# Performance work log

Hardware: AMD Instinct MI355X
Metric: run time of the kernel (lower is better)

## Reference

```python
import jax, jax.numpy as jnp
import numpy as np

N_NODES = 100000
N_CELLS = 200000
N_EDGES = 300000
D = 128            # input_size == attention_size
HID = 128          # hidden width of custom_func MLP
SCALE = np.sqrt(np.float32(D))


def segment_softmax(src, seg_ids, num_segments):
    # src: [M, 1], seg_ids: [M] -> softmax normalized within each segment
    m = jax.ops.segment_max(src, seg_ids, num_segments=num_segments)
    e = jnp.exp(src - m[seg_ids])
    s = jax.ops.segment_sum(e, seg_ids, num_segments=num_segments)
    return e / s[seg_ids]


def setup_inputs() -> dict:
    key = jax.random.key(0)
    ks = jax.random.split(key, 9)
    cell_attr = jax.random.normal(ks[0], (N_CELLS, D), dtype=jnp.float32)
    edge_attr = jax.random.normal(ks[1], (N_EDGES, D), dtype=jnp.float32)
    node_embedding = jax.random.normal(ks[2], (N_NODES, D), dtype=jnp.float32)
    edge_index = jax.random.randint(ks[3], (2, N_EDGES), 0, N_NODES, dtype=jnp.int32)
    face = jax.random.randint(ks[4], (3, N_CELLS), 0, N_NODES, dtype=jnp.int32)
    # custom_func: 2-layer MLP (2D -> HID -> D)
    W1 = jax.random.normal(ks[5], (2 * D, HID), dtype=jnp.float32) / np.sqrt(2 * D)
    b1 = jnp.zeros((HID,), dtype=jnp.float32)
    W2 = jax.random.normal(ks[6], (HID, D), dtype=jnp.float32) / np.sqrt(HID)
    b2 = jnp.zeros((D,), dtype=jnp.float32)
    return {"cell_attr": cell_attr, "edge_attr": edge_attr,
            "node_embedding": node_embedding, "edge_index": edge_index,
            "face": face, "W1": W1, "b1": b1, "W2": W2, "b2": b2}


def reference(cell_attr, edge_attr, node_embedding, edge_index, face, W1, b1, W2, b2):
    senders, receivers = edge_index[0], edge_index[1]
    two_out = jnp.concatenate([receivers, senders], axis=0)   # outdegree order [2E]
    two_edge = jnp.concatenate([edge_attr, edge_attr], axis=0)  # [2E, D]

    # attention over edges grouped by target (outdegree) node
    att_src = jnp.sum(two_edge * node_embedding[two_out], axis=1, keepdims=True) / SCALE
    att = segment_softmax(att_src, two_out, N_NODES)            # [2E, 1]
    node_agg = jax.ops.segment_sum(two_edge * att, two_out, num_segments=N_NODES)  # [N, D]

    # cells gather mean of their 3 nodes
    cell_agg = (node_agg[face[0]] + node_agg[face[1]] + node_agg[face[2]]) / 3.0  # [C, D]

    # custom_func MLP on cat(cell_attr, cell_agg)
    h = jax.nn.relu(jnp.concatenate([cell_attr, cell_agg], axis=1) @ W1 + b1)
    cell_attr_new = h @ W2 + b2                                  # [C, D]

    # scatter_mean of cell features back to nodes
    cells_node_index = jnp.concatenate([face[0], face[1], face[2]], axis=0)  # [3C]
    tripled = jnp.concatenate([cell_attr_new] * 3, axis=0)                   # [3C, D]
    sums = jax.ops.segment_sum(tripled, cells_node_index, num_segments=N_NODES)
    counts = jax.ops.segment_sum(jnp.ones((3 * N_CELLS,), jnp.float32),
                                 cells_node_index, num_segments=N_NODES)
    node_attr = sums / jnp.maximum(counts, 1.0)[:, None]

    return cell_attr_new, node_attr
```

## Files before the change

kernel.cpp:

```cpp
#include <hip/hip_runtime.h>

#define NN 100000
#define NC 200000
#define NE 300000
#define D  128
#define NB 391
#define HB 2344

typedef unsigned short u16;
typedef __attribute__((ext_vector_type(8))) short bf16x8;
typedef __attribute__((ext_vector_type(4))) float f32x4;

__device__ __forceinline__ u16 f2bf(float x) {
    unsigned int u = __float_as_uint(x);
    u += 0x7fffu + ((u >> 16) & 1u);
    return (u16)(u >> 16);
}
__device__ __forceinline__ float bf2f(u16 h) {
    return __uint_as_float((unsigned int)h << 16);
}
__device__ __forceinline__ unsigned int cvt_pk_bf16(float a, float b) {
    unsigned int r;
    asm("v_cvt_pk_bf16_f32 %0, %1, %2" : "=v"(r) : "v"(a), "v"(b));
    return r;
}

#define MFMA16(a, b, c) __builtin_amdgcn_mfma_f32_16x16x32_bf16((a), (b), (c), 0, 0, 0)

__global__ __launch_bounds__(256) void k_hist_w(const int* __restrict__ ei,
                                                const int* __restrict__ face,
                                                int* __restrict__ cntA,
                                                int* __restrict__ cntF,
                                                const float* __restrict__ W1,
                                                const float* __restrict__ W2,
                                                u16* __restrict__ w1h, u16* __restrict__ w1l,
                                                u16* __restrict__ w2h, u16* __restrict__ w2l) {
    int b = blockIdx.x;
    int t = threadIdx.x;
    if (b < HB) {
        int i = b * 256 + t;
        if (i >= 2 * NE) return;
        int tgt = (i < NE) ? ei[NE + i] : ei[i - NE];
        atomicAdd(&cntA[tgt], 1);
    } else if (b < 2 * HB) {
        int i = (b - HB) * 256 + t;
        if (i >= 3 * NC) return;
        atomicAdd(&cntF[face[i]], 1);
    } else {
        int tid = (b - 2 * HB) * 256 + t;
        if (tid >= 6144) return;
        int l = tid & 63;
        int f = tid >> 6;
        const float* W; u16 *oh, *ol; int fi;
        if (f < 64) { W = W1; oh = w1h; ol = w1l; fi = f; }
        else        { W = W2; oh = w2h; ol = w2l; fi = f - 64; }
        int kt = fi >> 3, nt = fi & 7;
        int k0 = kt * 32 + 8 * (l >> 4);
        int n  = nt * 16 + (l & 15);
        #pragma unroll
        for (int i = 0; i < 8; i++) {
            float x = W[(size_t)(k0 + i) * 128 + n];
            u16 h = f2bf(x);
            oh[(size_t)fi * 512 + l * 8 + i] = h;
            ol[(size_t)fi * 512 + l * 8 + i] = f2bf(x - bf2f(h));
        }
    }
}

__global__ __launch_bounds__(256) void k_scan_blocks(const int* __restrict__ cntA,
                                                     const int* __restrict__ cntF,
                                                     int* __restrict__ bsumA,
                                                     int* __restrict__ bsumF) {
    __shared__ int s[256];
    int bb = blockIdx.x;
    bool fa = bb >= NB;
    const int* cnt = fa ? cntF : cntA;
    int* bsum = fa ? bsumF : bsumA;
    int blk = fa ? bb - NB : bb;
    int t = threadIdx.x;
    int i = blk * 256 + t;
    s[t] = (i < NN) ? cnt[i] : 0;
    __syncthreads();
    #pragma unroll
    for (int off = 128; off > 0; off >>= 1) {
        if (t < off) s[t] += s[t + off];
        __syncthreads();
    }
    if (t == 0) bsum[blk] = s[0];
}

__global__ __launch_bounds__(512) void k_scan_top(int* __restrict__ bsumA,
                                                  int* __restrict__ bsumF, int nb) {
    __shared__ int s[512];
    int* bsum = blockIdx.x ? bsumF : bsumA;
    int t = threadIdx.x;
    int v = (t < nb) ? bsum[t] : 0;
    s[t] = v;
    __syncthreads();
    #pragma unroll
    for (int off = 1; off < 512; off <<= 1) {
        int x = (t >= off) ? s[t - off] : 0;
        __syncthreads();
        s[t] += x;
        __syncthreads();
    }
    if (t < nb) bsum[t] = s[t] - v;
}

__global__ __launch_bounds__(256) void k_scan_final(const int* __restrict__ cntA,
                                                    const int* __restrict__ cntF,
                                                    const int* __restrict__ bsumA,
                                                    const int* __restrict__ bsumF,
                                                    int* __restrict__ offA,
                                                    int* __restrict__ offF) {
    __shared__ int s[256];
    int bb = blockIdx.x;
    bool fa = bb >= NB;
    const int* cnt = fa ? cntF : cntA;
    const int* bsum = fa ? bsumF : bsumA;
    int* off_out = fa ? offF : offA;
    int total = fa ? 3 * NC : 2 * NE;
    int blk = fa ? bb - NB : bb;
    int t = threadIdx.x;
    int i = blk * 256 + t;
    int v = (i < NN) ? cnt[i] : 0;
    s[t] = v;
    __syncthreads();
    #pragma unroll
    for (int off = 1; off < 256; off <<= 1) {
        int x = (t >= off) ? s[t - off] : 0;
        __syncthreads();
        s[t] += x;
        __syncthreads();
    }
    if (i < NN) off_out[i] = s[t] - v + bsum[blk];
    if (i == 0) off_out[NN] = total;
}

__global__ __launch_bounds__(256) void k_fill(const int* __restrict__ ei,
                                              const int* __restrict__ face,
                                              const int* __restrict__ offA,
                                              const int* __restrict__ offF,
                                              int* __restrict__ curA,
                                              int* __restrict__ curF,
                                              int* __restrict__ slotsA,
                                              int* __restrict__ slotsF) {
    int b = blockIdx.x;
    int t = threadIdx.x;
    if (b < HB) {
        int i = b * 256 + t;
        if (i >= 2 * NE) return;
        int tgt = (i < NE) ? ei[NE + i] : ei[i - NE];
        int pos = offA[tgt] + atomicAdd(&curA[tgt], 1);
        slotsA[pos] = (i < NE) ? i : i - NE;
    } else {
        int i = (b - HB) * 256 + t;
        if (i >= 3 * NC) return;
        int tgt = face[i];
        int pos = offF[tgt] + atomicAdd(&curF[tgt], 1);
        int c = i; if (c >= NC) c -= NC; if (c >= NC) c -= NC;
        slotsF[pos] = c;
    }
}

__global__ __launch_bounds__(256) void k_agg_att(const float* __restrict__ edge_attr,
                                                 const float* __restrict__ emb,
                                                 const int* __restrict__ offs,
                                                 const int* __restrict__ slots,
                                                 float* __restrict__ na) {
    int n = blockIdx.x * 4 + (threadIdx.x >> 6);
    int lane = threadIdx.x & 63;
    if (n >= NN) return;
    int s0 = offs[n], s1 = offs[n + 1];
    int deg = s1 - s0;
    float2 e = ((const float2*)(emb + (size_t)n * D))[lane];
    const float inv_scale = 0.08838834764831845f;
    float2 acc = {0.f, 0.f};
    float wsum = 0.f;
    int base = 0;
    while (base < deg) {
        int chunk = deg - base;
        if (chunk > 64) chunk = 64;
        int sl = (lane < chunk) ? slots[s0 + base + lane] : 0;
        int j = 0;
        for (; j + 4 <= chunk; j += 4) {
            int r0 = __shfl(sl, j),     r1 = __shfl(sl, j + 1);
            int r2 = __shfl(sl, j + 2), r3 = __shfl(sl, j + 3);
            float2 a0 = ((const float2*)(edge_attr + (size_t)r0 * D))[lane];
            float2 a1 = ((const float2*)(edge_attr + (size_t)r1 * D))[lane];
            float2 a2 = ((const float2*)(edge_attr + (size_t)r2 * D))[lane];
            float2 a3 = ((const float2*)(edge_attr + (size_t)r3 * D))[lane];
            float d0 = a0.x * e.x + a0.y * e.y;
            float d1 = a1.x * e.x + a1.y * e.y;
            float d2 = a2.x * e.x + a2.y * e.y;
            float d3 = a3.x * e.x + a3.y * e.y;
            #pragma unroll
            for (int off = 32; off > 0; off >>= 1) {
                d0 += __shfl_xor(d0, off);
                d1 += __shfl_xor(d1, off);
                d2 += __shfl_xor(d2, off);
                d3 += __shfl_xor(d3, off);
            }
            float w0 = __expf(d0 * inv_scale);
            float w1 = __expf(d1 * inv_scale);
            float w2 = __expf(d2 * inv_scale);
            float w3 = __expf(d3 * inv_scale);
            acc.x += w0 * a0.x + w1 * a1.x + w2 * a2.x + w3 * a3.x;
            acc.y += w0 * a0.y + w1 * a1.y + w2 * a2.y + w3 * a3.y;
            wsum += (w0 + w1) + (w2 + w3);
        }
        for (; j < chunk; ++j) {
            int rr = __shfl(sl, j);
            float2 a = ((const float2*)(edge_attr + (size_t)rr * D))[lane];
            float d = a.x * e.x + a.y * e.y;
            #pragma unroll
            for (int off = 32; off > 0; off >>= 1) d += __shfl_xor(d, off);
            float w = __expf(d * inv_scale);
            acc.x += w * a.x;
            acc.y += w * a.y;
            wsum += w;
        }
        base += chunk;
    }
    float inv = (deg > 0) ? 1.f / wsum : 0.f;
    float2 r; r.x = acc.x * inv; r.y = acc.y * inv;
    ((float2*)(na + (size_t)n * D))[lane] = r;
}

__global__ __launch_bounds__(256) void k_smean_gather(const float* __restrict__ cell_out,
                                                      const int* __restrict__ offs,
                                                      const int* __restrict__ slots,
                                                      float* __restrict__ node_out) {
    int n = blockIdx.x * 4 + (threadIdx.x >> 6);
    int lane = threadIdx.x & 63;
    if (n >= NN) return;
    int s0 = offs[n], s1 = offs[n + 1];
    int deg = s1 - s0;
    float2 acc = {0.f, 0.f};
    int base = 0;
    while (base < deg) {
        int chunk = deg - base;
        if (chunk > 64) chunk = 64;
        int sl = 0;
        if (lane < chunk) sl = slots[s0 + base + lane];
        int j = 0;
        for (; j + 4 <= chunk; j += 4) {
            int c0 = __shfl(sl, j),     c1 = __shfl(sl, j + 1);
            int c2 = __shfl(sl, j + 2), c3 = __shfl(sl, j + 3);
            float2 y0 = ((const float2*)(cell_out + (size_t)c0 * D))[lane];
            float2 y1 = ((const float2*)(cell_out + (size_t)c1 * D))[lane];
            float2 y2 = ((const float2*)(cell_out + (size_t)c2 * D))[lane];
            float2 y3 = ((const float2*)(cell_out + (size_t)c3 * D))[lane];
            acc.x += y0.x + y1.x + y2.x + y3.x;
            acc.y += y0.y + y1.y + y2.y + y3.y;
        }
        for (; j < chunk; ++j) {
            int cc = __shfl(sl, j);
            float2 y = ((const float2*)(cell_out + (size_t)cc * D))[lane];
            acc.x += y.x;
            acc.y += y.y;
        }
        base += chunk;
    }
    float inv = deg ? 1.f / (float)deg : 0.f;
    float2 r; r.x = acc.x * inv; r.y = acc.y * inv;
    ((float2*)(node_out + (size_t)n * D))[lane] = r;
}

__device__ __forceinline__ void stage_split(char* lds, int row, int col8, const float* v) {
    unsigned int byte = ((unsigned int)row << 9) + ((unsigned int)col8 << 4);
    byte ^= (unsigned int)(row & 7) << 4;
    uint4 hi, lo;
    unsigned int* hp = (unsigned int*)&hi;
    unsigned int* lp = (unsigned int*)&lo;
    #pragma unroll
    for (int i = 0; i < 4; i++) {
        unsigned int h = cvt_pk_bf16(v[2 * i], v[2 * i + 1]);
        float h0 = __uint_as_float(h << 16);
        float h1 = __uint_as_float(h & 0xffff0000u);
        hp[i] = h;
        lp[i] = cvt_pk_bf16(v[2 * i] - h0, v[2 * i + 1] - h1);
    }
    *(uint4*)(lds + byte)         = hi;
    *(uint4*)(lds + 16384 + byte) = lo;
}

__global__ __launch_bounds__(256, 5) void k_mlp(const float* __restrict__ cell_attr,
                                                const float* __restrict__ na,
                                                const int* __restrict__ face,
                                                const u16* __restrict__ w1h,
                                                const u16* __restrict__ w1l,
                                                const u16* __restrict__ w2h,
                                                const u16* __restrict__ w2l,
                                                const float* __restrict__ b1,
                                                const float* __restrict__ b2,
                                                float* __restrict__ out) {
    __shared__ char lds[32768];
    const int t  = threadIdx.x;
    const int c0 = blockIdx.x * 32;

    {
        const int r = t >> 3;
        const int q = t & 7;
        float v[16];
        const float* pa = cell_attr + (size_t)(c0 + r) * D + q * 16;
        #pragma unroll
        for (int i = 0; i < 4; i++) *(float4*)(v + 4 * i) = *(const float4*)(pa + 4 * i);
        stage_split(lds, r, q * 2,     v);
        stage_split(lds, r, q * 2 + 1, v + 8);

        const int cid = c0 + r;
        const int f0 = face[cid], f1 = face[NC + cid], f2 = face[2 * NC + cid];
        const float* p0 = na + (size_t)f0 * D + q * 16;
        const float* p1 = na + (size_t)f1 * D + q * 16;
        const float* p2 = na + (size_t)f2 * D + q * 16;
        const float third = 1.f / 3.f;
        #pragma unroll
        for (int i = 0; i < 4; i++) {
            float4 a0 = *(const float4*)(p0 + 4 * i);
            float4 a1 = *(const float4*)(p1 + 4 * i);
            float4 a2 = *(const float4*)(p2 + 4 * i);
            v[4 * i + 0] = (a0.x + a1.x + a2.x) * third;
            v[4 * i + 1] = (a0.y + a1.y + a2.y) * third;
            v[4 * i + 2] = (a0.z + a1.z + a2.z) * third;
            v[4 * i + 3] = (a0.w + a1.w + a2.w) * third;
        }
        stage_split(lds, r, 16 + q * 2, v);
        stage_split(lds, r, 17 + q * 2, v + 8);
    }
    __syncthreads();

    const int w  = t >> 6;
    const int l  = t & 63;
    const int lr = l & 15;
    const int lg = l >> 4;
    const unsigned int swz = (unsigned int)(lr & 7) << 4;
    const size_t wl8 = (size_t)l * 8;
    const f32x4 z4 = {0.f, 0.f, 0.f, 0.f};
    f32x4 acc[2][2] = {{z4, z4}, {z4, z4}};

    {
        const unsigned int abase = ((unsigned int)lr << 9) + ((unsigned int)lg << 4);
        const u16* pW1h = w1h + (size_t)(w * 2) * 512 + wl8;
        const u16* pW1l = w1l + (size_t)(w * 2) * 512 + wl8;
        #pragma unroll 2
        for (int kt = 0; kt < 8; ++kt) {
            unsigned int ab = (abase + (unsigned int)kt * 64) ^ swz;
            bf16x8 aH0 = *(const bf16x8*)(lds + ab);
            bf16x8 aL0 = *(const bf16x8*)(lds + 16384 + ab);
            bf16x8 aH1 = *(const bf16x8*)(lds + ab + 8192);
            bf16x8 aL1 = *(const bf16x8*)(lds + 16384 + ab + 8192);
            #pragma unroll
            for (int jn = 0; jn < 2; ++jn) {
                size_t fo = (size_t)(kt * 8 + jn) * 512;
                bf16x8 bH = *(const bf16x8*)(pW1h + fo);
                bf16x8 bL = *(const bf16x8*)(pW1l + fo);
                acc[0][jn] = MFMA16(aH0, bL, acc[0][jn]);
                acc[0][jn] = MFMA16(aL0, bH, acc[0][jn]);
                acc[0][jn] = MFMA16(aH0, bH, acc[0][jn]);
                acc[1][jn] = MFMA16(aH1, bL, acc[1][jn]);
                acc[1][jn] = MFMA16(aL1, bH, acc[1][jn]);
                acc[1][jn] = MFMA16(aH1, bH, acc[1][jn]);
            }
        }
    }

    __syncthreads();

    {
        const int col0 = w * 32 + lr;
        const int col1 = col0 + 16;
        const float bb0 = b1[col0];
        const float bb1 = b1[col1];
        #pragma unroll
        for (int rt = 0; rt < 2; ++rt) {
            #pragma unroll
            for (int r = 0; r < 4; ++r) {
                int row = rt * 16 + lg * 4 + r;
                float h0 = fmaxf(acc[rt][0][r] + bb0, 0.f);
                float h1 = fmaxf(acc[rt][1][r] + bb1, 0.f);
                unsigned int ph = cvt_pk_bf16(h0, h1);
                float f0 = __uint_as_float(ph << 16);
                float f1 = __uint_as_float(ph & 0xffff0000u);
                unsigned int pl = cvt_pk_bf16(h0 - f0, h1 - f1);
                unsigned int swzr = (unsigned int)(row & 7) << 4;
                unsigned int b0 = (((unsigned int)row << 8) + ((unsigned int)col0 << 1)) ^ swzr;
                unsigned int bcol1 = (((unsigned int)row << 8) + ((unsigned int)col1 << 1)) ^ swzr;
                *(u16*)(lds + b0)            = (u16)ph;
                *(u16*)(lds + bcol1)         = (u16)(ph >> 16);
                *(u16*)(lds + 8192 + b0)     = (u16)pl;
                *(u16*)(lds + 8192 + bcol1)  = (u16)(pl >> 16);
            }
        }
    }
    __syncthreads();

    f32x4 acc2[2][2] = {{z4, z4}, {z4, z4}};
    {
        const unsigned int abase = ((unsigned int)lr << 8) + ((unsigned int)lg << 4);
        const u16* pW2h = w2h + (size_t)(w * 2) * 512 + wl8;
        const u16* pW2l = w2l + (size_t)(w * 2) * 512 + wl8;
        #pragma unroll 2
        for (int kt = 0; kt < 4; ++kt) {
            unsigned int ab = (abase + (unsigned int)kt * 64) ^ swz;
            bf16x8 aH0 = *(const bf16x8*)(lds + ab);
            bf16x8 aL0 = *(const bf16x8*)(lds + 8192 + ab);
            bf16x8 aH1 = *(const bf16x8*)(lds + ab + 4096);
            bf16x8 aL1 = *(const bf16x8*)(lds + 8192 + ab + 4096);
            #pragma unroll
            for (int jn = 0; jn < 2; ++jn) {
                size_t fo = (size_t)(kt * 8 + jn) * 512;
                bf16x8 bH = *(const bf16x8*)(pW2h + fo);
                bf16x8 bL = *(const bf16x8*)(pW2l + fo);
                acc2[0][jn] = MFMA16(aH0, bL, acc2[0][jn]);
                acc2[0][jn] = MFMA16(aL0, bH, acc2[0][jn]);
                acc2[0][jn] = MFMA16(aH0, bH, acc2[0][jn]);
                acc2[1][jn] = MFMA16(aH1, bL, acc2[1][jn]);
                acc2[1][jn] = MFMA16(aL1, bH, acc2[1][jn]);
                acc2[1][jn] = MFMA16(aH1, bH, acc2[1][jn]);
            }
        }
    }

    #pragma unroll
    for (int jn = 0; jn < 2; ++jn) {
        int col = w * 32 + jn * 16 + lr;
        float bb = b2[col];
        #pragma unroll
        for (int rt = 0; rt < 2; ++rt) {
            #pragma unroll
            for (int r = 0; r < 4; ++r) {
                int row = c0 + rt * 16 + lg * 4 + r;
                out[(size_t)row * D + col] = acc2[rt][jn][r] + bb;
            }
        }
    }
}

extern "C" void kernel_launch(void* const* d_in, const int* in_sizes, int n_in,
                              void* d_out, int out_size, void* d_ws, size_t ws_size,
                              hipStream_t stream) {
    (void)in_sizes; (void)n_in; (void)out_size; (void)ws_size;
    const float* cell_attr = (const float*)d_in[0];
    const float* edge_attr = (const float*)d_in[1];
    const float* emb       = (const float*)d_in[2];
    const int*   ei        = (const int*)d_in[3];
    const int*   face      = (const int*)d_in[4];
    const float* W1        = (const float*)d_in[5];
    const float* b1        = (const float*)d_in[6];
    const float* W2        = (const float*)d_in[7];
    const float* b2        = (const float*)d_in[8];

    float* out_cell = (float*)d_out;
    float* out_node = out_cell + (size_t)NC * D;

    int*   cntA   = (int*)d_ws;
    int*   cntF   = cntA + NN;
    int*   curA   = cntF + NN;
    int*   curF   = curA + NN;
    int*   offA   = curF + NN;
    int*   offF   = offA + NN + 1;
    int*   bsumA  = offF + NN + 1;
    int*   bsumF  = bsumA + 512;
    int*   slotsA = bsumF + 512;
    int*   slotsF = slotsA + 2 * NE;
    u16* w1h = (u16*)(((uintptr_t)(slotsF + 3 * NC) + 15) & ~(uintptr_t)15);
    u16* w1l = w1h + 64 * 512;
    u16* w2h = w1l + 64 * 512;
    u16* w2l = w2h + 32 * 512;

    hipMemsetAsync(d_ws, 0, (size_t)4 * NN * 4, stream);

    k_hist_w<<<2 * HB + 24, 256, 0, stream>>>(ei, face, cntA, cntF, W1, W2,
                                              w1h, w1l, w2h, w2l);

    k_scan_blocks<<<2 * NB, 256, 0, stream>>>(cntA, cntF, bsumA, bsumF);
    k_scan_top   <<<2, 512, 0, stream>>>(bsumA, bsumF, NB);
    k_scan_final <<<2 * NB, 256, 0, stream>>>(cntA, cntF, bsumA, bsumF, offA, offF);

    k_fill<<<2 * HB, 256, 0, stream>>>(ei, face, offA, offF, curA, curF, slotsA, slotsF);

    k_agg_att<<<(NN + 3) / 4, 256, 0, stream>>>(edge_attr, emb, offA, slotsA, out_node);

    k_mlp<<<NC / 32, 256, 0, stream>>>(cell_attr, out_node, face,
                                       w1h, w1l, w2h, w2l, b1, b2, out_cell);

    k_smean_gather<<<(NN + 3) / 4, 256, 0, stream>>>(out_cell, offF, slotsF, out_node);
}
```

Measured before the change: 639.6 us.

## Gather bf16 copies of edge and cell features; overlap MLP node gather with GEMM

Adds a bf16 conversion of edge_attr, done inside the histogram kernel, so the attention aggregation gathers half the bytes per edge. The MLP now also writes a bf16 copy of its output, which the scatter-mean gather reads in place of fp32. In the MLP, loads of node aggregates are issued before the first half of GEMM1 and staged after it to hide latency, and the launch-bounds occupancy hint drops from 5 to 4. The costs are an extra conversion pass and extra writes, reduced precision in the attention and mean outputs, and a dependence on there being enough workspace for both bf16 buffers.

After: 676.9 us. 5.8% more time.

```diff
diff --git a/kernel.cpp b/kernel.cpp
--- a/kernel.cpp
+++ b/kernel.cpp
@@ -6,6 +6,7 @@
 #define D  128
 #define NB 391
 #define HB 2344
+#define ECB 9375
 
 typedef unsigned short u16;
 typedef __attribute__((ext_vector_type(8))) short bf16x8;
@@ -29,12 +30,14 @@
 
 __global__ __launch_bounds__(256) void k_hist_w(const int* __restrict__ ei,
                                                 const int* __restrict__ face,
+                                                const float* __restrict__ edge_attr,
                                                 int* __restrict__ cntA,
                                                 int* __restrict__ cntF,
                                                 const float* __restrict__ W1,
                                                 const float* __restrict__ W2,
                                                 u16* __restrict__ w1h, u16* __restrict__ w1l,
-                                                u16* __restrict__ w2h, u16* __restrict__ w2l) {
+                                                u16* __restrict__ w2h, u16* __restrict__ w2l,
+                                                u16* __restrict__ eab) {
     int b = blockIdx.x;
     int t = threadIdx.x;
     if (b < HB) {
@@ -46,7 +49,7 @@
         int i = (b - HB) * 256 + t;
         if (i >= 3 * NC) return;
         atomicAdd(&cntF[face[i]], 1);
-    } else {
+    } else if (b < 2 * HB + 24) {
         int tid = (b - 2 * HB) * 256 + t;
         if (tid >= 6144) return;
         int l = tid & 63;
@@ -64,6 +67,19 @@
             oh[(size_t)fi * 512 + l * 8 + i] = h;
             ol[(size_t)fi * 512 + l * 8 + i] = f2bf(x - bf2f(h));
         }
+    } else {
+        size_t base = ((size_t)(b - 2 * HB - 24) * 256 + t) * 16;
+        const float4* src = (const float4*)(edge_attr + base);
+        uint4 o[2];
+        unsigned int* op = (unsigned int*)o;
+        #pragma unroll
+        for (int i = 0; i < 4; i++) {
+            float4 v4 = src[i];
+            op[2 * i]     = cvt_pk_bf16(v4.x, v4.y);
+            op[2 * i + 1] = cvt_pk_bf16(v4.z, v4.w);
+        }
+        ((uint4*)(eab + base))[0] = o[0];
+        ((uint4*)(eab + base))[1] = o[1];
     }
 }
 
@@ -163,7 +179,20 @@
     }
 }
 
+template<int BF>
+__device__ __forceinline__ float2 erow(const float* ea, const u16* eb, int row, int lane) {
+    if (BF) {
+        unsigned int u = ((const unsigned int*)(eb + (size_t)row * D))[lane];
+        float2 r; r.x = bf2f((u16)(u & 0xffffu)); r.y = bf2f((u16)(u >> 16));
+        return r;
+    } else {
+        return ((const float2*)(ea + (size_t)row * D))[lane];
+    }
+}
+
+template<int BF>
 __global__ __launch_bounds__(256) void k_agg_att(const float* __restrict__ edge_attr,
+                                                 const u16* __restrict__ eab,
                                                  const float* __restrict__ emb,
                                                  const int* __restrict__ offs,
                                                  const int* __restrict__ slots,
@@ -186,10 +215,10 @@
         for (; j + 4 <= chunk; j += 4) {
             int r0 = __shfl(sl, j),     r1 = __shfl(sl, j + 1);
             int r2 = __shfl(sl, j + 2), r3 = __shfl(sl, j + 3);
-            float2 a0 = ((const float2*)(edge_attr + (size_t)r0 * D))[lane];
-            float2 a1 = ((const float2*)(edge_attr + (size_t)r1 * D))[lane];
-            float2 a2 = ((const float2*)(edge_attr + (size_t)r2 * D))[lane];
-            float2 a3 = ((const float2*)(edge_attr + (size_t)r3 * D))[lane];
+            float2 a0 = erow<BF>(edge_attr, eab, r0, lane);
+            float2 a1 = erow<BF>(edge_attr, eab, r1, lane);
+            float2 a2 = erow<BF>(edge_attr, eab, r2, lane);
+            float2 a3 = erow<BF>(edge_attr, eab, r3, lane);
             float d0 = a0.x * e.x + a0.y * e.y;
             float d1 = a1.x * e.x + a1.y * e.y;
             float d2 = a2.x * e.x + a2.y * e.y;
@@ -211,7 +240,7 @@
         }
         for (; j < chunk; ++j) {
             int rr = __shfl(sl, j);
-            float2 a = ((const float2*)(edge_attr + (size_t)rr * D))[lane];
+            float2 a = erow<BF>(edge_attr, eab, rr, lane);
             float d = a.x * e.x + a.y * e.y;
             #pragma unroll
             for (int off = 32; off > 0; off >>= 1) d += __shfl_xor(d, off);
@@ -227,7 +256,9 @@
     ((float2*)(na + (size_t)n * D))[lane] = r;
 }
 
+template<int BF>
 __global__ __launch_bounds__(256) void k_smean_gather(const float* __restrict__ cell_out,
+                                                      const u16* __restrict__ cob,
                                                       const int* __restrict__ offs,
                                                       const int* __restrict__ slots,
                                                       float* __restrict__ node_out) {
@@ -247,16 +278,16 @@
         for (; j + 4 <= chunk; j += 4) {
             int c0 = __shfl(sl, j),     c1 = __shfl(sl, j + 1);
             int c2 = __shfl(sl, j + 2), c3 = __shfl(sl, j + 3);
-            float2 y0 = ((const float2*)(cell_out + (size_t)c0 * D))[lane];
-            float2 y1 = ((const float2*)(cell_out + (size_t)c1 * D))[lane];
-            float2 y2 = ((const float2*)(cell_out + (size_t)c2 * D))[lane];
-            float2 y3 = ((const float2*)(cell_out + (size_t)c3 * D))[lane];
+            float2 y0 = erow<BF>(cell_out, cob, c0, lane);
+            float2 y1 = erow<BF>(cell_out, cob, c1, lane);
+            float2 y2 = erow<BF>(cell_out, cob, c2, lane);
+            float2 y3 = erow<BF>(cell_out, cob, c3, lane);
             acc.x += y0.x + y1.x + y2.x + y3.x;
             acc.y += y0.y + y1.y + y2.y + y3.y;
         }
         for (; j < chunk; ++j) {
             int cc = __shfl(sl, j);
-            float2 y = ((const float2*)(cell_out + (size_t)cc * D))[lane];
+            float2 y = erow<BF>(cell_out, cob, cc, lane);
             acc.x += y.x;
             acc.y += y.y;
         }
@@ -285,7 +316,7 @@
     *(uint4*)(lds + 16384 + byte) = lo;
 }
 
-__global__ __launch_bounds__(256, 5) void k_mlp(const float* __restrict__ cell_attr,
+__global__ __launch_bounds__(256, 4) void k_mlp(const float* __restrict__ cell_attr,
                                                 const float* __restrict__ na,
                                                 const int* __restrict__ face,
                                                 const u16* __restrict__ w1h,
@@ -294,39 +325,32 @@
                                                 const u16* __restrict__ w2l,
                                                 const float* __restrict__ b1,
                                                 const float* __restrict__ b2,
-                                                float* __restrict__ out) {
+                                                float* __restrict__ out,
+                                                u16* __restrict__ cob) {
     __shared__ char lds[32768];
     const int t  = threadIdx.x;
     const int c0 = blockIdx.x * 32;
+    const int r  = t >> 3;
+    const int q  = t & 7;
 
     {
-        const int r = t >> 3;
-        const int q = t & 7;
         float v[16];
         const float* pa = cell_attr + (size_t)(c0 + r) * D + q * 16;
         #pragma unroll
         for (int i = 0; i < 4; i++) *(float4*)(v + 4 * i) = *(const float4*)(pa + 4 * i);
         stage_split(lds, r, q * 2,     v);
         stage_split(lds, r, q * 2 + 1, v + 8);
-
+    }
+
+    float4 n0[4], n1[4], n2[4];
+    {
         const int cid = c0 + r;
         const int f0 = face[cid], f1 = face[NC + cid], f2 = face[2 * NC + cid];
-        const float* p0 = na + (size_t)f0 * D + q * 16;
-        const float* p1 = na + (size_t)f1 * D + q * 16;
-        const float* p2 = na + (size_t)f2 * D + q * 16;
-        const float third = 1.f / 3.f;
-        #pragma unroll
-        for (int i = 0; i < 4; i++) {
-            float4 a0 = *(const float4*)(p0 + 4 * i);
-            float4 a1 = *(const float4*)(p1 + 4 * i);
-            float4 a2 = *(const float4*)(p2 + 4 * i);
-            v[4 * i + 0] = (a0.x + a1.x + a2.x) * third;
-            v[4 * i + 1] = (a0.y + a1.y + a2.y) * third;
-            v[4 * i + 2] = (a0.z + a1.z + a2.z) * third;
-            v[4 * i + 3] = (a0.w + a1.w + a2.w) * third;
-        }
-        stage_split(lds, r, 16 + q * 2, v);
-        stage_split(lds, r, 17 + q * 2, v + 8);
+        const float4* p0 = (const float4*)(na + (size_t)f0 * D + q * 16);
+        const float4* p1 = (const float4*)(na + (size_t)f1 * D + q * 16);
+        const float4* p2 = (const float4*)(na + (size_t)f2 * D + q * 16);
+        #pragma unroll
+        for (int i = 0; i < 4; i++) { n0[i] = p0[i]; n1[i] = p1[i]; n2[i] = p2[i]; }
     }
     __syncthreads();
 
@@ -339,13 +363,13 @@
     const f32x4 z4 = {0.f, 0.f, 0.f, 0.f};
     f32x4 acc[2][2] = {{z4, z4}, {z4, z4}};
 
-    {
-        const unsigned int abase = ((unsigned int)lr << 9) + ((unsigned int)lg << 4);
-        const u16* pW1h = w1h + (size_t)(w * 2) * 512 + wl8;
-        const u16* pW1l = w1l + (size_t)(w * 2) * 512 + wl8;
+    const unsigned int abase1 = ((unsigned int)lr << 9) + ((unsigned int)lg << 4);
+    const u16* pW1h = w1h + (size_t)(w * 2) * 512 + wl8;
+    const u16* pW1l = w1l + (size_t)(w * 2) * 512 + wl8;
+    auto gemm1 = [&](int ktb, int kte) {
         #pragma unroll 2
-        for (int kt = 0; kt < 8; ++kt) {
-            unsigned int ab = (abase + (unsigned int)kt * 64) ^ swz;
+        for (int kt = ktb; kt < kte; ++kt) {
+            unsigned int ab = (abase1 + (unsigned int)kt * 64) ^ swz;
             bf16x8 aH0 = *(const bf16x8*)(lds + ab);
             bf16x8 aL0 = *(const bf16x8*)(lds + 16384 + ab);
             bf16x8 aH1 = *(const bf16x8*)(lds + ab + 8192);
@@ -363,7 +387,26 @@
                 acc[1][jn] = MFMA16(aH1, bH, acc[1][jn]);
             }
         }
-    }
+    };
+
+    gemm1(0, 4);
+
+    {
+        float v[16];
+        const float third = 1.f / 3.f;
+        #pragma unroll
+        for (int i = 0; i < 4; i++) {
+            v[4 * i + 0] = (n0[i].x + n1[i].x + n2[i].x) * third;
+            v[4 * i + 1] = (n0[i].y + n1[i].y + n2[i].y) * third;
+            v[4 * i + 2] = (n0[i].z + n1[i].z + n2[i].z) * third;
+            v[4 * i + 3] = (n0[i].w + n1[i].w + n2[i].w) * third;
+        }
+        stage_split(lds, r, 16 + q * 2, v);
+        stage_split(lds, r, 17 + q * 2, v + 8);
+    }
+    __syncthreads();
+
+    gemm1(4, 8);
 
     __syncthreads();
 
@@ -375,10 +418,10 @@
         #pragma unroll
         for (int rt = 0; rt < 2; ++rt) {
             #pragma unroll
-            for (int r = 0; r < 4; ++r) {
-                int row = rt * 16 + lg * 4 + r;
-                float h0 = fmaxf(acc[rt][0][r] + bb0, 0.f);
-                float h1 = fmaxf(acc[rt][1][r] + bb1, 0.f);
+            for (int rr = 0; rr < 4; ++rr) {
+                int row = rt * 16 + lg * 4 + rr;
+                float h0 = fmaxf(acc[rt][0][rr] + bb0, 0.f);
+                float h1 = fmaxf(acc[rt][1][rr] + bb1, 0.f);
                 unsigned int ph = cvt_pk_bf16(h0, h1);
                 float f0 = __uint_as_float(ph << 16);
                 float f1 = __uint_as_float(ph & 0xffff0000u);
@@ -429,9 +472,11 @@
         #pragma unroll
         for (int rt = 0; rt < 2; ++rt) {
             #pragma unroll
-            for (int r = 0; r < 4; ++r) {
-                int row = c0 + rt * 16 + lg * 4 + r;
-                out[(size_t)row * D + col] = acc2[rt][jn][r] + bb;
+            for (int rr = 0; rr < 4; ++rr) {
+                int row = c0 + rt * 16 + lg * 4 + rr;
+                float y = acc2[rt][jn][rr] + bb;
+                out[(size_t)row * D + col] = y;
+                if (cob) cob[(size_t)row * D + col] = f2bf(y);
             }
         }
     }
@@ -440,7 +485,7 @@
 extern "C" void kernel_launch(void* const* d_in, const int* in_sizes, int n_in,
                               void* d_out, int out_size, void* d_ws, size_t ws_size,
                               hipStream_t stream) {
-    (void)in_sizes; (void)n_in; (void)out_size; (void)ws_size;
+    (void)in_sizes; (void)n_in; (void)out_size;
     const float* cell_attr = (const float*)d_in[0];
     const float* edge_attr = (const float*)d_in[1];
     const float* emb       = (const float*)d_in[2];
@@ -468,11 +513,16 @@
     u16* w1l = w1h + 64 * 512;
     u16* w2h = w1l + 64 * 512;
     u16* w2l = w2h + 32 * 512;
+    u16* cob = (u16*)(((uintptr_t)(w2l + 32 * 512) + 255) & ~(uintptr_t)255);
+    u16* eab = (u16*)(((uintptr_t)(cob + (size_t)NC * D) + 255) & ~(uintptr_t)255);
+    const char* ws_end = (const char*)d_ws + ws_size;
+    bool has_cob = ((const char*)(cob + (size_t)NC * D) <= ws_end);
+    bool has_eab = ((const char*)(eab + (size_t)NE * D) <= ws_end);
 
     hipMemsetAsync(d_ws, 0, (size_t)4 * NN * 4, stream);
 
-    k_hist_w<<<2 * HB + 24, 256, 0, stream>>>(ei, face, cntA, cntF, W1, W2,
-                                              w1h, w1l, w2h, w2l);
+    k_hist_w<<<2 * HB + 24 + (has_eab ? ECB : 0), 256, 0, stream>>>(
+        ei, face, edge_attr, cntA, cntF, W1, W2, w1h, w1l, w2h, w2l, eab);
 
     k_scan_blocks<<<2 * NB, 256, 0, stream>>>(cntA, cntF, bsumA, bsumF);
     k_scan_top   <<<2, 512, 0, stream>>>(bsumA, bsumF, NB);
@@ -480,10 +530,17 @@
 
     k_fill<<<2 * HB, 256, 0, stream>>>(ei, face, offA, offF, curA, curF, slotsA, slotsF);
 
-    k_agg_att<<<(NN + 3) / 4, 256, 0, stream>>>(edge_attr, emb, offA, slotsA, out_node);
+    if (has_eab)
+        k_agg_att<1><<<(NN + 3) / 4, 256, 0, stream>>>(edge_attr, eab, emb, offA, slotsA, out_node);
+    else
+        k_agg_att<0><<<(NN + 3) / 4, 256, 0, stream>>>(edge_attr, eab, emb, offA, slotsA, out_node);
 
     k_mlp<<<NC / 32, 256, 0, stream>>>(cell_attr, out_node, face,
-                                       w1h, w1l, w2h, w2l, b1, b2, out_cell);
-
-    k_smean_gather<<<(NN + 3) / 4, 256, 0, stream>>>(out_cell, offF, slotsF, out_node);
-}
+                                       w1h, w1l, w2h, w2l, b1, b2, out_cell,
+                                       has_cob ? cob : (u16*)nullptr);
+
+    if (has_cob)
+        k_smean_gather<1><<<(NN + 3) / 4, 256, 0, stream>>>(out_cell, cob, offF, slotsF, out_node);
+    else
+        k_smean_gather<0><<<(NN + 3) / 4, 256, 0, stream>>>(out_cell, cob, offF, slotsF, out_node);
+}
```
